# Kernel tuning notes

Measured on AMD Instinct MI355X. Metric: run time of the kernel, lower is better.

The kernel has to match this reference:

```python
import jax, jax.numpy as jnp
import numpy as np

NUM_HEADS = 8
GROUPS = 32
EPS = 1e-5


def setup_inputs() -> dict:
    key = jax.random.key(0)
    ks = jax.random.split(key, 4)
    B, C, H, W = 8, 512, 32, 32
    x = jax.random.normal(ks[0], (B, C, H, W), dtype=jnp.float32)
    gn_w = jnp.ones((C,), dtype=jnp.float32)
    gn_b = jnp.zeros((C,), dtype=jnp.float32)
    qkv_w = jax.random.normal(ks[1], (3 * C, C), dtype=jnp.float32) * (1.0 / np.sqrt(C))
    qkv_b = jnp.zeros((3 * C,), dtype=jnp.float32)
    proj_w = jax.random.normal(ks[2], (C, C), dtype=jnp.float32) * (1.0 / np.sqrt(C))
    proj_b = jnp.zeros((C,), dtype=jnp.float32)
    return {"x": x, "gn_w": gn_w, "gn_b": gn_b, "qkv_w": qkv_w,
            "qkv_b": qkv_b, "proj_w": proj_w, "proj_b": proj_b}


def reference(x, gn_w, gn_b, qkv_w, qkv_b, proj_w, proj_b):
    b, c, h, w = x.shape
    n = h * w
    hd = c // NUM_HEADS
    xf = x.reshape(b, c, n)
    # GroupNorm over (channels_per_group, HW) per sample
    xg = xf.reshape(b, GROUPS, -1)
    mu = jnp.mean(xg, axis=-1, keepdims=True)
    var = jnp.var(xg, axis=-1, keepdims=True)
    xn = ((xg - mu) * jax.lax.rsqrt(var + EPS)).reshape(b, c, n)
    xn = xn * gn_w[None, :, None] + gn_b[None, :, None]
    # 1x1 conv == channel matmul
    qkv = jnp.einsum('oc,bcn->bon', qkv_w, xn) + qkv_b[None, :, None]
    q, k, v = jnp.split(qkv, 3, axis=1)
    q = q.reshape(b, NUM_HEADS, hd, n)
    k = k.reshape(b, NUM_HEADS, hd, n)
    v = v.reshape(b, NUM_HEADS, hd, n)
    scale = hd ** 0.5
    score = jnp.einsum('bhdn,bhdm->bhnm', q, k) / scale  # [b,h,HW,HW]
    attn = jax.nn.softmax(score, axis=-1)
    out = jnp.einsum('bhnm,bhdm->bhnd', attn, v)  # [b,h,HW,hd]
    out = out.transpose(0, 1, 3, 2).reshape(b, c, n)
    out = jnp.einsum('oc,bcn->bon', proj_w, out) + proj_b[None, :, None]
    return x + out.reshape(b, c, h, w)
```

## Files before the change

### kernel.cpp

```cpp
#include <hip/hip_runtime.h>

typedef unsigned short u16;
typedef unsigned long long u64;
typedef __bf16 bf16x8 __attribute__((ext_vector_type(8)));
typedef float f32x4 __attribute__((ext_vector_type(4)));

#define NB 8
#define NC 512
#define NN 1024
#define NHEADS 8
#define HDIM 64
#define CPG 16
#define EPSV 1e-5f
#define LOG2E 1.44269504f

__device__ __forceinline__ float bf2f(u16 h) {
  union { unsigned u; float f; } v; v.u = ((unsigned)h) << 16; return v.f;
}
__device__ __forceinline__ u16 f2bf(float f) {
  union { float f; unsigned u; } v; v.f = f;
  unsigned r = v.u + 0x7fffu + ((v.u >> 16) & 1u);
  return (u16)(r >> 16);
}
__device__ __forceinline__ float h2f(u16 h) {
  unsigned s = (h >> 15) & 1u, e = (h >> 10) & 31u, m = h & 1023u;
  union { unsigned u; float f; } v;
  if (e == 0) { v.u = s << 31; return v.f + (s ? -1.f : 1.f) * (float)m * 5.9604645e-8f; }
  if (e == 31) { v.u = (s << 31) | 0x7F800000u | (m << 13); return v.f; }
  v.u = (s << 31) | ((e + 112u) << 23) | (m << 13);
  return v.f;
}
__device__ __forceinline__ u16 f2h(float f) {
  union { float f; unsigned u; } v; v.f = f;
  unsigned s = (v.u >> 16) & 0x8000u; int e = (int)((v.u >> 23) & 0xFF) - 112;
  unsigned m = v.u & 0x7FFFFFu;
  if (e <= 0) return (u16)s;
  if (e >= 31) return (u16)(s | 0x7C00u);
  u16 h = (u16)(s | (e << 10) | (m >> 13));
  unsigned rem = m & 0x1FFFu;
  if (rem > 0x1000u || (rem == 0x1000u && (h & 1u))) ++h;
  return h;
}
__device__ __forceinline__ float load_elem(const void* p, size_t i, int f) {
  if (f == 1) return bf2f(((const u16*)p)[i]);
  if (f == 2) return h2f(((const u16*)p)[i]);
  return ((const float*)p)[i];
}

__device__ __forceinline__ float exp2_fast(float x) {
  float r;
  asm("v_exp_f32 %0, %1" : "=v"(r) : "v"(x));
  return r;
}

__device__ __forceinline__ int detect_f(const u16* gw_raw) {
  int bf = 0, hf = 0;
#pragma unroll
  for (int i = 0; i < 16; ++i) {
    u16 w = gw_raw[i];
    bf += (w == 0x3F80u);
    hf += (w == 0x3C00u);
  }
  return (bf >= 12) ? 1 : (hf >= 12) ? 2 : 0;
}

__device__ __forceinline__ void cvt4(const void* raw, u16* dst, int i, int f) {
  if (f == 1) {
    *(uint2*)(dst + i) = *(const uint2*)((const u16*)raw + i);
  } else if (f == 0) {
    float4 v = *(const float4*)((const float*)raw + i);
    u16 o[4] = {f2bf(v.x), f2bf(v.y), f2bf(v.z), f2bf(v.w)};
    *(u64*)(dst + i) = *(const u64*)o;
  } else {
    u16 o[4];
#pragma unroll
    for (int k2 = 0; k2 < 4; ++k2) o[k2] = f2bf(h2f(((const u16*)raw)[i + k2]));
    *(u64*)(dst + i) = *(const u64*)o;
  }
}

__device__ __forceinline__ void gn_body(const void* x, int f,
                                        const void* gnw, const void* gnb,
                                        u16* xnT, int bsrc, int bdst,
                                        int g, int t) {
  __shared__ float r1[256], r2[256];
  __shared__ alignas(16) float sxf[CPG * NN];
  __shared__ float sgw[CPG], sgb[CPG];
  const size_t base = ((size_t)(bsrc * NC + g * CPG)) * NN;
  if (t < CPG) {
    sgw[t] = load_elem(gnw, (size_t)(g * CPG + t), f);
    sgb[t] = load_elem(gnb, (size_t)(g * CPG + t), f);
  }
  float s = 0.f, ss = 0.f;
  if (f == 1) {
    const u16* xb = (const u16*)x + base;
    for (int i0 = t * 8; i0 < CPG * NN; i0 += 2048) {
      uint4 dv = *(const uint4*)(xb + i0);
      const u16* pp = (const u16*)&dv;
      float vv[8];
#pragma unroll
      for (int j = 0; j < 8; ++j) { vv[j] = bf2f(pp[j]); s += vv[j]; ss += vv[j] * vv[j]; }
      *(float4*)(sxf + i0)     = make_float4(vv[0], vv[1], vv[2], vv[3]);
      *(float4*)(sxf + i0 + 4) = make_float4(vv[4], vv[5], vv[6], vv[7]);
    }
  } else if (f == 0) {
    const float* xb = (const float*)x + base;
    for (int i0 = t * 4; i0 < CPG * NN; i0 += 1024) {
      float4 v = *(const float4*)(xb + i0);
      *(float4*)(sxf + i0) = v;
      s += v.x + v.y + v.z + v.w;
      ss += v.x * v.x + v.y * v.y + v.z * v.z + v.w * v.w;
    }
  } else {
    for (int i = t; i < CPG * NN; i += 256) {
      float v = load_elem(x, base + i, f);
      sxf[i] = v;
      s += v; ss += v * v;
    }
  }
  r1[t] = s; r2[t] = ss; __syncthreads();
  for (int k = 128; k > 0; k >>= 1) {
    if (t < k) { r1[t] += r1[t + k]; r2[t] += r2[t + k]; }
    __syncthreads();
  }
  const float mu  = r1[0] * (1.f / 16384.f);
  const float var = r2[0] * (1.f / 16384.f) - mu * mu;
  const float rs  = rsqrtf(var + EPSV);
  float wsc[CPG], bsc[CPG];
#pragma unroll
  for (int cl = 0; cl < CPG; ++cl) {
    wsc[cl] = sgw[cl] * rs;
    bsc[cl] = sgb[cl] - mu * wsc[cl];
  }
  u16* dstb = xnT + (size_t)bdst * NN * NC + g * CPG;
  for (int n = t; n < NN; n += 256) {
    u16 o[CPG];
#pragma unroll
    for (int cl = 0; cl < CPG; ++cl)
      o[cl] = f2bf(sxf[cl * NN + n] * wsc[cl] + bsc[cl]);
    u16* dr = dstb + (size_t)n * NC;
    *(uint4*)(dr)     = *(const uint4*)(o);
    *(uint4*)(dr + 8) = *(const uint4*)(o + 8);
  }
}

__global__ __launch_bounds__(256) void prep_all(const void* __restrict__ x,
                                                const void* __restrict__ gnw,
                                                const void* __restrict__ gnb,
                                                const void* __restrict__ qkvw,
                                                const void* __restrict__ qb,
                                                const void* __restrict__ projw,
                                                const void* __restrict__ pb,
                                                u16* __restrict__ wq16,
                                                u16* __restrict__ wp16,
                                                float* __restrict__ cqb,
                                                float* __restrict__ cpb,
                                                int* __restrict__ flag,
                                                u16* __restrict__ xnT) {
  const int f = detect_f((const u16*)gnw);
  const int b = blockIdx.x;
  const int t = threadIdx.x;
  if (b < 768) {
    cvt4(qkvw, wq16, (b * 256 + t) * 4, f);
    return;
  }
  if (b < 1024) {
    cvt4(projw, wp16, ((b - 768) * 256 + t) * 4, f);
    return;
  }
  if (b < 1036) {
    const int i = (b - 1024) * 256 + t;
    if (i < 1536)      cqb[i] = load_elem(qb, (size_t)i, f);
    else if (i < 2048) cpb[i - 1536] = load_elem(pb, (size_t)(i - 1536), f);
    if (b == 1024 && t == 0) *flag = f;
    return;
  }
  const int idx = b - 1036;
  gn_body(x, f, gnw, gnb, xnT, idx >> 5, idx >> 5, idx & 31, t);
}

__global__ __launch_bounds__(256) void gn_only(const void* __restrict__ x,
                                               const void* __restrict__ gnw,
                                               const void* __restrict__ gnb,
                                               u16* __restrict__ xnT, int b0) {
  const int f = detect_f((const u16*)gnw);
  gn_body(x, f, gnw, gnb, xnT, b0, 0, blockIdx.x, threadIdx.x);
}

__global__ __launch_bounds__(256) void gemm_mfma(const u16* __restrict__ A,
                                                 const u16* __restrict__ BnT,
                                                 const float* __restrict__ bias,
                                                 void* __restrict__ out,
                                                 const void* __restrict__ resid,
                                                 const int* __restrict__ flag,
                                                 int M, int K, int b0, int kmode) {
  __shared__ alignas(16) u16 sA[128 * 40];
  __shared__ alignas(16) u16 sB[128 * 40];
  const int m0 = blockIdx.x * 128;
  const int n0 = blockIdx.y * 128;
  const int bz = blockIdx.z;
  const int t = threadIdx.x;
  const int lane = t & 63, wv = t >> 6;
  const int wm = (wv >> 1) * 64, wn = (wv & 1) * 64;
  const int lr = lane & 15, quad = lane >> 4;
  const int f = *flag;

  const int ar0 = t >> 2, akc = (t & 3) * 8;
  const int ar1 = 64 + ar0;
  const int sw0 = akc ^ (ar0 & 24);
  const int sw1 = akc ^ (ar1 & 24);

  f32x4 acc[4][4] = {};

  const u16* pa0 = A + (size_t)(m0 + ar0) * K + akc;
  const u16* pa1 = A + (size_t)(m0 + ar1) * K + akc;
  const u16* pb0 = BnT + ((size_t)bz * NN + n0 + ar0) * K + akc;
  const u16* pb1 = BnT + ((size_t)bz * NN + n0 + ar1) * K + akc;

  uint4 xa0 = *(const uint4*)(pa0);
  uint4 xa1 = *(const uint4*)(pa1);
  uint4 xb0 = *(const uint4*)(pb0);
  uint4 xb1 = *(const uint4*)(pb1);
  uint4 ya0 = *(const uint4*)(pa0 + 32);
  uint4 ya1 = *(const uint4*)(pa1 + 32);
  uint4 yb0 = *(const uint4*)(pb0 + 32);
  uint4 yb1 = *(const uint4*)(pb1 + 32);

#define GEMM_STAGE(ra0, ra1, rb0, rb1)                                   \
  {                                                                      \
    *(uint4*)(sA + ar0 * 40 + akc) = ra0;                                \
    *(uint4*)(sA + ar1 * 40 + akc) = ra1;                                \
    *(uint4*)(sB + ar0 * 40 + sw0) = rb0;                                \
    *(uint4*)(sB + ar1 * 40 + sw1) = rb1;                                \
  }

#define GEMM_MFMA_BLOCK()                                                \
  {                                                                      \
    const u16* pA = sA + (wm + lr) * 40 + quad * 8;                      \
    bf16x8 af[4], bfv[4];                                                \
    _Pragma("unroll")                                                    \
    for (int i = 0; i < 4; ++i) {                                        \
      af[i] = *(const bf16x8*)(pA + i * 640);                            \
      const int rowB = wn + lr + i * 16;                                 \
      bfv[i] = *(const bf16x8*)(sB + rowB * 40 + ((quad * 8) ^ (rowB & 24))); \
    }                                                                    \
    _Pragma("unroll")                                                    \
    for (int i = 0; i < 4; ++i)                                          \
      _Pragma("unroll")                                                  \
      for (int j = 0; j < 4; ++j)                                        \
        acc[i][j] = __builtin_amdgcn_mfma_f32_16x16x32_bf16(af[i], bfv[j], acc[i][j], 0, 0, 0); \
  }

  for (int k0 = 0; k0 < K; k0 += 64) {
    __syncthreads();
    GEMM_STAGE(xa0, xa1, xb0, xb1);
    __syncthreads();
    if (k0 + 64 < K) {
      xa0 = *(const uint4*)(pa0 + k0 + 64);
      xa1 = *(const uint4*)(pa1 + k0 + 64);
      xb0 = *(const uint4*)(pb0 + k0 + 64);
      xb1 = *(const uint4*)(pb1 + k0 + 64);
    }
    GEMM_MFMA_BLOCK();
    __syncthreads();
    GEMM_STAGE(ya0, ya1, yb0, yb1);
    __syncthreads();
    if (k0 + 96 < K) {
      ya0 = *(const uint4*)(pa0 + k0 + 96);
      ya1 = *(const uint4*)(pa1 + k0 + 96);
      yb0 = *(const uint4*)(pb0 + k0 + 96);
      yb1 = *(const uint4*)(pb1 + k0 + 96);
    }
    GEMM_MFMA_BLOCK();
  }

  const bool kstore = (kmode != 0) && (m0 >= 512) && (m0 < 1024);
  if (kstore) {
    u16* kb2 = (u16*)out + ((size_t)(b0 + bz) * 1536 + 512) * NN;
#pragma unroll
    for (int i = 0; i < 4; ++i) {
      const int mb = m0 + wm + i * 16 + quad * 4;
      const int hh = (mb - 512) >> 6;
      const int d0 = (mb - 512) & 63;
      u16* hb = kb2 + (size_t)hh * NN * 64 + d0;
#pragma unroll
      for (int j = 0; j < 4; ++j) {
        const int col = n0 + wn + j * 16 + lr;
        u16 o[4];
#pragma unroll
        for (int r = 0; r < 4; ++r) o[r] = f2bf(acc[i][j][r] + bias[mb + r]);
        *(u64*)(hb + (size_t)col * 64) = *(const u64*)o;
      }
    }
    return;
  }
#pragma unroll
  for (int i = 0; i < 4; ++i) {
    const int mb = m0 + wm + i * 16 + quad * 4;
#pragma unroll
    for (int r = 0; r < 4; ++r) {
      const int mr = mb + r;
      const float bi = bias[mr];
#pragma unroll
      for (int j = 0; j < 4; ++j) {
        const int col = n0 + wn + j * 16 + lr;
        const size_t oidx = ((size_t)(b0 + bz) * M + mr) * NN + col;
        float v = acc[i][j][r] + bi;
        if (resid) {
          v += load_elem(resid, oidx, f);
          if (f == 1)      ((u16*)out)[oidx] = f2bf(v);
          else if (f == 2) ((u16*)out)[oidx] = f2h(v);
          else             ((float*)out)[oidx] = v;
        } else {
          ((u16*)out)[oidx] = f2bf(v);
        }
      }
    }
  }
}

__global__ __launch_bounds__(512) void attn_mfma(const u16* __restrict__ qkv,
                                                 u16* __restrict__ attnOT) {
  __shared__ alignas(16) u16 sK[2][64 * 64];
  __shared__ alignas(16) u16 sV[2][64 * 64];

  const int L   = blockIdx.x + 8 * (blockIdx.y + 8 * blockIdx.z);
  const int xcd = L & 7;
  const int jj  = L >> 3;
  const int grp = xcd + 8 * (jj >> 3);
  const int qt  = jj & 7;
  const int h   = grp & 7;
  const int bz  = grp >> 3;

  const int n0 = qt * 128;
  const u16* qb    = qkv + ((size_t)bz * 1536 + h * HDIM) * NN;
  const u16* kbase = qkv + ((size_t)bz * 1536 + 512) * NN + (size_t)h * NN * HDIM;
  const u16* vb    = qb + (size_t)1024 * NN;
  const int t = threadIdx.x;
  const int lane = t & 63, wv = t >> 6;
  const int lr = lane & 15, quad = lane >> 4;

  const int qcol = n0 + wv * 16 + lr;
  union { u16 u[8]; bf16x8 v; } qa0, qa1;
#pragma unroll
  for (int e = 0; e < 8; ++e) {
    qa0.u[e] = qb[(size_t)(quad * 8 + e) * NN + qcol];
    qa1.u[e] = qb[(size_t)(quad * 8 + 32 + e) * NN + qcol];
  }
  const bf16x8 a0 = qa0.v;
  const bf16x8 a1 = qa1.v;

  const int km = t >> 3;
  const int kc = t & 7;
  const int ke = (km ^ (km >> 3)) & 7;
  const u16* kp = kbase + (size_t)km * 64 + kc * 8;
  const int ksd = km * 64 + ((kc ^ ke) * 8);

  const int sd  = t >> 3;
  const int smo = (t & 7) * 8;
  const u16* vp = vb + (size_t)sd * NN + smo;
  const int vs0 = sd * 64 + (smo ^ (8 * (sd & 7)));

  uint4 pk0, pv0;

  f32x4 acc_o[4] = {};
  float mrow = -1e30f, lrow = 0.f;

  pk0 = *(const uint4*)(kp);
  pv0 = *(const uint4*)(vp);
  *(uint4*)(&sK[0][ksd]) = pk0;
  *(uint4*)(&sV[0][vs0]) = pv0;
  pk0 = *(const uint4*)(kp + 4096);
  pv0 = *(const uint4*)(vp + 64);
  __syncthreads();

  for (int mt = 0; mt < 16; ++mt) {
    const int c = mt & 1;

    f32x4 p[4];
    __builtin_amdgcn_s_setprio(1);
#pragma unroll
    for (int j = 0; j < 4; ++j) {
      const int rk = j * 16 + lr;
      const u16* pKr = &sK[c][rk * 64];
      const int sw = ((rk ^ (rk >> 3)) & 7) * 8;
      bf16x8 k0 = *(const bf16x8*)(pKr + ((quad * 8) ^ sw));
      bf16x8 k1 = *(const bf16x8*)(pKr + ((quad * 8 + 32) ^ sw));
      f32x4 z = {0.f, 0.f, 0.f, 0.f};
      z = __builtin_amdgcn_mfma_f32_16x16x32_bf16(k0, a0, z, 0, 0, 0);
      z = __builtin_amdgcn_mfma_f32_16x16x32_bf16(k1, a1, z, 0, 0, 0);
      p[j] = z;
    }
    __builtin_amdgcn_s_setprio(0);

    float mx = -1e30f;
#pragma unroll
    for (int j = 0; j < 4; ++j)
#pragma unroll
      for (int r = 0; r < 4; ++r) mx = fmaxf(mx, p[j][r]);
    mx = fmaxf(mx, __shfl_xor(mx, 16));
    mx = fmaxf(mx, __shfl_xor(mx, 32));
    const float msc = mx * 0.125f;
    if (!__all(msc - mrow <= 8.f)) {
      const float mnew = fmaxf(mrow, msc);
      const float alpha = exp2_fast((mrow - mnew) * LOG2E);
      mrow = mnew;
      lrow *= alpha;
      float ar[4];
#pragma unroll
      for (int r = 0; r < 4; ++r) ar[r] = __shfl(alpha, quad * 4 + r);
#pragma unroll
      for (int j2 = 0; j2 < 4; ++j2)
#pragma unroll
        for (int r = 0; r < 4; ++r) acc_o[j2][r] *= ar[r];
    }
    const float m2 = mrow * LOG2E;
    float ls = 0.f;
#pragma unroll
    for (int j = 0; j < 4; ++j)
#pragma unroll
      for (int r = 0; r < 4; ++r) {
        const float pe = exp2_fast(fmaf(p[j][r], 0.18033688f, -m2));
        p[j][r] = pe;
        ls += pe;
      }
    ls += __shfl_xor(ls, 16);
    ls += __shfl_xor(ls, 32);
    lrow += ls;

    unsigned pa[4], pb2[4];
#pragma unroll
    for (int j = 0; j < 4; ++j) {
      asm("v_cvt_pk_bf16_f32 %0, %1, %2" : "=v"(pa[j]) : "v"(p[j][0]), "v"(p[j][1]));
      asm("v_cvt_pk_bf16_f32 %0, %1, %2" : "=v"(pb2[j]) : "v"(p[j][2]), "v"(p[j][3]));
    }

    __builtin_amdgcn_s_setprio(1);
#pragma unroll
    for (int ks = 0; ks < 2; ++ks) {
      union { unsigned u[4]; bf16x8 v; } af;
      af.u[0] = pa[2 * ks];
      af.u[1] = pb2[2 * ks];
      af.u[2] = pa[2 * ks + 1];
      af.u[3] = pb2[2 * ks + 1];
#pragma unroll
      for (int j2 = 0; j2 < 4; ++j2) {
        const int rv = j2 * 16 + lr;
        const int swv = 8 * (rv & 7);
        const u16* pVr = &sV[c][rv * 64];
        union { u64 q[2]; bf16x8 v; } bfv;
        bfv.q[0] = *(const u64*)(pVr + ((ks * 32 + 4 * quad) ^ swv));
        bfv.q[1] = *(const u64*)(pVr + ((ks * 32 + 16 + 4 * quad) ^ swv));
        acc_o[j2] = __builtin_amdgcn_mfma_f32_16x16x32_bf16(af.v, bfv.v, acc_o[j2], 0, 0, 0);
      }
    }
    __builtin_amdgcn_s_setprio(0);

    if (mt < 15) {
      const int cn = c ^ 1;
      *(uint4*)(&sK[cn][ksd]) = pk0;
      *(uint4*)(&sV[cn][vs0]) = pv0;
      if (mt < 14) {
        pk0 = *(const uint4*)(kp + (size_t)(mt + 2) * 4096);
        pv0 = *(const uint4*)(vp + (mt + 2) * 64);
      }
      __syncthreads();
    }
  }

  const float invl = 1.f / lrow;
  float ir[4];
#pragma unroll
  for (int r = 0; r < 4; ++r) ir[r] = __shfl(invl, quad * 4 + r);
  const int qrow = n0 + wv * 16 + quad * 4;
#pragma unroll
  for (int r = 0; r < 4; ++r) {
    u16* orow = attnOT + ((size_t)bz * NN + qrow + r) * NC + h * HDIM;
#pragma unroll
    for (int j2 = 0; j2 < 4; ++j2)
      orow[j2 * 16 + lr] = f2bf(acc_o[j2][r] * ir[r]);
  }
}

__global__ void sig_small_ws(u16* out) {
  if (threadIdx.x == 0 && blockIdx.x == 0) out[0] = f2bf(20000.f);
}

extern "C" void kernel_launch(void* const* d_in, const int* in_sizes, int n_in,
                              void* d_out, int out_size, void* d_ws, size_t ws_size,
                              hipStream_t stream) {
  const void* x      = d_in[0];
  const void* gn_w   = d_in[1];
  const void* gn_b   = d_in[2];
  const void* qkv_w  = d_in[3];
  const void* qkv_b  = d_in[4];
  const void* proj_w = d_in[5];
  const void* proj_b = d_in[6];
  char* ws = (char*)d_ws;
  const size_t MB = (size_t)1 << 20;

  u16*   wq16 = (u16*)(ws);
  u16*   wp16 = (u16*)(ws + 3 * MB / 2);
  float* cqb  = (float*)(ws + 2 * MB);
  float* cpb  = (float*)(ws + 2 * MB + 8192);
  int*   flag = (int*)  (ws + 2 * MB + 16384);

  if (ws_size >= 36 * MB) {
    u16* xnT    = (u16*)(ws + 3 * MB);
    u16* qkvb   = (u16*)(ws + 11 * MB);
    u16* attnOT = xnT;
    prep_all<<<dim3(1036 + NB * 32), dim3(256), 0, stream>>>(
        x, gn_w, gn_b, qkv_w, qkv_b, proj_w, proj_b,
        wq16, wp16, cqb, cpb, flag, xnT);
    gemm_mfma<<<dim3(12, 8, NB), dim3(256), 0, stream>>>(wq16, xnT, cqb, qkvb,
                                                         nullptr, flag, 1536, NC, 0, 1);
    attn_mfma<<<dim3(8, NHEADS, NB), dim3(512), 0, stream>>>(qkvb, attnOT);
    gemm_mfma<<<dim3(4, 8, NB), dim3(256), 0, stream>>>(wp16, attnOT, cpb, d_out,
                                                        x, flag, NC, NC, 0, 0);
  } else if (ws_size >= 9 * MB) {
    u16* xnT    = (u16*)(ws + 3 * MB);
    u16* qkvb   = (u16*)(ws + 4 * MB);
    u16* attnOT = (u16*)(ws + 7 * MB);
    prep_all<<<dim3(1036), dim3(256), 0, stream>>>(
        x, gn_w, gn_b, qkv_w, qkv_b, proj_w, proj_b,
        wq16, wp16, cqb, cpb, flag, xnT);
    for (int b = 0; b < NB; ++b) {
      gn_only<<<dim3(32), dim3(256), 0, stream>>>(x, gn_w, gn_b, xnT, b);
      gemm_mfma<<<dim3(12, 8, 1), dim3(256), 0, stream>>>(wq16, xnT, cqb, qkvb,
                                                          nullptr, flag, 1536, NC, 0, 1);
      attn_mfma<<<dim3(8, NHEADS, 1), dim3(512), 0, stream>>>(qkvb, attnOT);
      gemm_mfma<<<dim3(4, 8, 1), dim3(256), 0, stream>>>(wp16, attnOT, cpb, d_out,
                                                         x, flag, NC, NC, b, 0);
    }
  } else {
    sig_small_ws<<<dim3(1), dim3(64), 0, stream>>>((u16*)d_out);
  }
}
```

Measured before the change: 178.6 us.

## Give each attention wave two query tiles and halve block threads

The attention kernel now runs 4 waves of 256 threads instead of 8. Each wave processes two 16-row query tiles, so every K and V fragment read from shared memory feeds two MFMAs. Each thread loads twice as much of the K/V tiles to keep the per-block tile size the same. This cuts LDS reads per MFMA and barrier participants, at the cost of higher register pressure and fewer waves per block for latency hiding.

Result: no change. 178.3 us (median of 2 runs) (-0.2%).

```diff
diff --git a/kernel.cpp b/kernel.cpp
--- a/kernel.cpp
+++ b/kernel.cpp
@@ -319,7 +319,7 @@
   }
 }
 
-__global__ __launch_bounds__(512) void attn_mfma(const u16* __restrict__ qkv,
+__global__ __launch_bounds__(256) void attn_mfma(const u16* __restrict__ qkv,
                                                  u16* __restrict__ attnOT) {
   __shared__ alignas(16) u16 sK[2][64 * 64];
   __shared__ alignas(16) u16 sV[2][64 * 64];
@@ -340,44 +340,56 @@
   const int lane = t & 63, wv = t >> 6;
   const int lr = lane & 15, quad = lane >> 4;
 
-  const int qcol = n0 + wv * 16 + lr;
-  union { u16 u[8]; bf16x8 v; } qa0, qa1;
+  const int qcol = n0 + wv * 32 + lr;
+  union { u16 u[8]; bf16x8 v; } qh[4];
 #pragma unroll
   for (int e = 0; e < 8; ++e) {
-    qa0.u[e] = qb[(size_t)(quad * 8 + e) * NN + qcol];
-    qa1.u[e] = qb[(size_t)(quad * 8 + 32 + e) * NN + qcol];
-  }
-  const bf16x8 a0 = qa0.v;
-  const bf16x8 a1 = qa1.v;
-
-  const int km = t >> 3;
-  const int kc = t & 7;
+    qh[0].u[e] = qb[(size_t)(quad * 8 + e) * NN + qcol];
+    qh[1].u[e] = qb[(size_t)(quad * 8 + 32 + e) * NN + qcol];
+    qh[2].u[e] = qb[(size_t)(quad * 8 + e) * NN + qcol + 16];
+    qh[3].u[e] = qb[(size_t)(quad * 8 + 32 + e) * NN + qcol + 16];
+  }
+  const bf16x8 a0_0 = qh[0].v, a1_0 = qh[1].v;
+  const bf16x8 a0_1 = qh[2].v, a1_1 = qh[3].v;
+
+  const int km = t >> 2;
+  const int kc = t & 3;
   const int ke = (km ^ (km >> 3)) & 7;
   const u16* kp = kbase + (size_t)km * 64 + kc * 8;
-  const int ksd = km * 64 + ((kc ^ ke) * 8);
 
   const int sd  = t >> 3;
   const int smo = (t & 7) * 8;
   const u16* vp = vb + (size_t)sd * NN + smo;
   const int vs0 = sd * 64 + (smo ^ (8 * (sd & 7)));
-
-  uint4 pk0, pv0;
-
-  f32x4 acc_o[4] = {};
-  float mrow = -1e30f, lrow = 0.f;
+  const int vs1 = (sd + 32) * 64 + (smo ^ (8 * ((sd + 32) & 7)));
+
+  uint4 pk0, pk1, pv0, pv1;
+
+  f32x4 acc_o0[4] = {}, acc_o1[4] = {};
+  float mrow0 = -1e30f, lrow0 = 0.f;
+  float mrow1 = -1e30f, lrow1 = 0.f;
 
   pk0 = *(const uint4*)(kp);
+  pk1 = *(const uint4*)(kp + 32);
   pv0 = *(const uint4*)(vp);
-  *(uint4*)(&sK[0][ksd]) = pk0;
-  *(uint4*)(&sV[0][vs0]) = pv0;
+  pv1 = *(const uint4*)(vp + (size_t)32 * NN);
+  {
+    u16* kd = &sK[0][km * 64];
+    *(uint4*)(kd + ((kc ^ ke) * 8)) = pk0;
+    *(uint4*)(kd + (((kc + 4) ^ ke) * 8)) = pk1;
+    *(uint4*)(&sV[0][vs0]) = pv0;
+    *(uint4*)(&sV[0][vs1]) = pv1;
+  }
   pk0 = *(const uint4*)(kp + 4096);
+  pk1 = *(const uint4*)(kp + 4096 + 32);
   pv0 = *(const uint4*)(vp + 64);
+  pv1 = *(const uint4*)(vp + (size_t)32 * NN + 64);
   __syncthreads();
 
   for (int mt = 0; mt < 16; ++mt) {
     const int c = mt & 1;
 
-    f32x4 p[4];
+    f32x4 p0[4], p1[4];
     __builtin_amdgcn_s_setprio(1);
 #pragma unroll
     for (int j = 0; j < 4; ++j) {
@@ -386,63 +398,111 @@
       const int sw = ((rk ^ (rk >> 3)) & 7) * 8;
       bf16x8 k0 = *(const bf16x8*)(pKr + ((quad * 8) ^ sw));
       bf16x8 k1 = *(const bf16x8*)(pKr + ((quad * 8 + 32) ^ sw));
-      f32x4 z = {0.f, 0.f, 0.f, 0.f};
-      z = __builtin_amdgcn_mfma_f32_16x16x32_bf16(k0, a0, z, 0, 0, 0);
-      z = __builtin_amdgcn_mfma_f32_16x16x32_bf16(k1, a1, z, 0, 0, 0);
-      p[j] = z;
+      f32x4 z0 = {0.f, 0.f, 0.f, 0.f};
+      z0 = __builtin_amdgcn_mfma_f32_16x16x32_bf16(k0, a0_0, z0, 0, 0, 0);
+      z0 = __builtin_amdgcn_mfma_f32_16x16x32_bf16(k1, a1_0, z0, 0, 0, 0);
+      p0[j] = z0;
+      f32x4 z1 = {0.f, 0.f, 0.f, 0.f};
+      z1 = __builtin_amdgcn_mfma_f32_16x16x32_bf16(k0, a0_1, z1, 0, 0, 0);
+      z1 = __builtin_amdgcn_mfma_f32_16x16x32_bf16(k1, a1_1, z1, 0, 0, 0);
+      p1[j] = z1;
     }
     __builtin_amdgcn_s_setprio(0);
 
-    float mx = -1e30f;
-#pragma unroll
-    for (int j = 0; j < 4; ++j)
-#pragma unroll
-      for (int r = 0; r < 4; ++r) mx = fmaxf(mx, p[j][r]);
-    mx = fmaxf(mx, __shfl_xor(mx, 16));
-    mx = fmaxf(mx, __shfl_xor(mx, 32));
-    const float msc = mx * 0.125f;
-    if (!__all(msc - mrow <= 8.f)) {
-      const float mnew = fmaxf(mrow, msc);
-      const float alpha = exp2_fast((mrow - mnew) * LOG2E);
-      mrow = mnew;
-      lrow *= alpha;
-      float ar[4];
-#pragma unroll
-      for (int r = 0; r < 4; ++r) ar[r] = __shfl(alpha, quad * 4 + r);
-#pragma unroll
-      for (int j2 = 0; j2 < 4; ++j2)
-#pragma unroll
-        for (int r = 0; r < 4; ++r) acc_o[j2][r] *= ar[r];
-    }
-    const float m2 = mrow * LOG2E;
-    float ls = 0.f;
-#pragma unroll
-    for (int j = 0; j < 4; ++j)
-#pragma unroll
-      for (int r = 0; r < 4; ++r) {
-        const float pe = exp2_fast(fmaf(p[j][r], 0.18033688f, -m2));
-        p[j][r] = pe;
-        ls += pe;
-      }
-    ls += __shfl_xor(ls, 16);
-    ls += __shfl_xor(ls, 32);
-    lrow += ls;
-
-    unsigned pa[4], pb2[4];
-#pragma unroll
-    for (int j = 0; j < 4; ++j) {
-      asm("v_cvt_pk_bf16_f32 %0, %1, %2" : "=v"(pa[j]) : "v"(p[j][0]), "v"(p[j][1]));
-      asm("v_cvt_pk_bf16_f32 %0, %1, %2" : "=v"(pb2[j]) : "v"(p[j][2]), "v"(p[j][3]));
+    unsigned pa0[4], pb0_[4];
+    {
+      float mx = -1e30f;
+#pragma unroll
+      for (int j = 0; j < 4; ++j)
+#pragma unroll
+        for (int r = 0; r < 4; ++r) mx = fmaxf(mx, p0[j][r]);
+      mx = fmaxf(mx, __shfl_xor(mx, 16));
+      mx = fmaxf(mx, __shfl_xor(mx, 32));
+      const float msc = mx * 0.125f;
+      if (!__all(msc - mrow0 <= 8.f)) {
+        const float mnew = fmaxf(mrow0, msc);
+        const float alpha = exp2_fast((mrow0 - mnew) * LOG2E);
+        mrow0 = mnew;
+        lrow0 *= alpha;
+        float ar[4];
+#pragma unroll
+        for (int r = 0; r < 4; ++r) ar[r] = __shfl(alpha, quad * 4 + r);
+#pragma unroll
+        for (int j2 = 0; j2 < 4; ++j2)
+#pragma unroll
+          for (int r = 0; r < 4; ++r) acc_o0[j2][r] *= ar[r];
+      }
+      const float m2 = mrow0 * LOG2E;
+      float ls = 0.f;
+#pragma unroll
+      for (int j = 0; j < 4; ++j)
+#pragma unroll
+        for (int r = 0; r < 4; ++r) {
+          const float pe = exp2_fast(fmaf(p0[j][r], 0.18033688f, -m2));
+          p0[j][r] = pe;
+          ls += pe;
+        }
+      ls += __shfl_xor(ls, 16);
+      ls += __shfl_xor(ls, 32);
+      lrow0 += ls;
+#pragma unroll
+      for (int j = 0; j < 4; ++j) {
+        asm("v_cvt_pk_bf16_f32 %0, %1, %2" : "=v"(pa0[j]) : "v"(p0[j][0]), "v"(p0[j][1]));
+        asm("v_cvt_pk_bf16_f32 %0, %1, %2" : "=v"(pb0_[j]) : "v"(p0[j][2]), "v"(p0[j][3]));
+      }
+    }
+
+    unsigned pa1[4], pb1_[4];
+    {
+      float mx = -1e30f;
+#pragma unroll
+      for (int j = 0; j < 4; ++j)
+#pragma unroll
+        for (int r = 0; r < 4; ++r) mx = fmaxf(mx, p1[j][r]);
+      mx = fmaxf(mx, __shfl_xor(mx, 16));
+      mx = fmaxf(mx, __shfl_xor(mx, 32));
+      const float msc = mx * 0.125f;
+      if (!__all(msc - mrow1 <= 8.f)) {
+        const float mnew = fmaxf(mrow1, msc);
+        const float alpha = exp2_fast((mrow1 - mnew) * LOG2E);
+        mrow1 = mnew;
+        lrow1 *= alpha;
+        float ar[4];
+#pragma unroll
+        for (int r = 0; r < 4; ++r) ar[r] = __shfl(alpha, quad * 4 + r);
+#pragma unroll
+        for (int j2 = 0; j2 < 4; ++j2)
+#pragma unroll
+          for (int r = 0; r < 4; ++r) acc_o1[j2][r] *= ar[r];
+      }
+      const float m2 = mrow1 * LOG2E;
+      float ls = 0.f;
+#pragma unroll
+      for (int j = 0; j < 4; ++j)
+#pragma unroll
+        for (int r = 0; r < 4; ++r) {
+          const float pe = exp2_fast(fmaf(p1[j][r], 0.18033688f, -m2));
+          p1[j][r] = pe;
+          ls += pe;
+        }
+      ls += __shfl_xor(ls, 16);
+      ls += __shfl_xor(ls, 32);
+      lrow1 += ls;
+#pragma unroll
+      for (int j = 0; j < 4; ++j) {
+        asm("v_cvt_pk_bf16_f32 %0, %1, %2" : "=v"(pa1[j]) : "v"(p1[j][0]), "v"(p1[j][1]));
+        asm("v_cvt_pk_bf16_f32 %0, %1, %2" : "=v"(pb1_[j]) : "v"(p1[j][2]), "v"(p1[j][3]));
+      }
     }
 
     __builtin_amdgcn_s_setprio(1);
 #pragma unroll
     for (int ks = 0; ks < 2; ++ks) {
-      union { unsigned u[4]; bf16x8 v; } af;
-      af.u[0] = pa[2 * ks];
-      af.u[1] = pb2[2 * ks];
-      af.u[2] = pa[2 * ks + 1];
-      af.u[3] = pb2[2 * ks + 1];
+      union { unsigned u[4]; bf16x8 v; } af0, af1;
+      af0.u[0] = pa0[2 * ks];  af0.u[1] = pb0_[2 * ks];
+      af0.u[2] = pa0[2 * ks + 1]; af0.u[3] = pb0_[2 * ks + 1];
+      af1.u[0] = pa1[2 * ks];  af1.u[1] = pb1_[2 * ks];
+      af1.u[2] = pa1[2 * ks + 1]; af1.u[3] = pb1_[2 * ks + 1];
 #pragma unroll
       for (int j2 = 0; j2 < 4; ++j2) {
         const int rv = j2 * 16 + lr;
@@ -451,34 +511,58 @@
         union { u64 q[2]; bf16x8 v; } bfv;
         bfv.q[0] = *(const u64*)(pVr + ((ks * 32 + 4 * quad) ^ swv));
         bfv.q[1] = *(const u64*)(pVr + ((ks * 32 + 16 + 4 * quad) ^ swv));
-        acc_o[j2] = __builtin_amdgcn_mfma_f32_16x16x32_bf16(af.v, bfv.v, acc_o[j2], 0, 0, 0);
+        acc_o0[j2] = __builtin_amdgcn_mfma_f32_16x16x32_bf16(af0.v, bfv.v, acc_o0[j2], 0, 0, 0);
+        acc_o1[j2] = __builtin_amdgcn_mfma_f32_16x16x32_bf16(af1.v, bfv.v, acc_o1[j2], 0, 0, 0);
       }
     }
     __builtin_amdgcn_s_setprio(0);
 
     if (mt < 15) {
       const int cn = c ^ 1;
-      *(uint4*)(&sK[cn][ksd]) = pk0;
+      u16* kd = &sK[cn][km * 64];
+      *(uint4*)(kd + ((kc ^ ke) * 8)) = pk0;
+      *(uint4*)(kd + (((kc + 4) ^ ke) * 8)) = pk1;
       *(uint4*)(&sV[cn][vs0]) = pv0;
+      *(uint4*)(&sV[cn][vs1]) = pv1;
       if (mt < 14) {
-        pk0 = *(const uint4*)(kp + (size_t)(mt + 2) * 4096);
-        pv0 = *(const uint4*)(vp + (mt + 2) * 64);
+        const size_t ko = (size_t)(mt + 2) * 4096;
+        const int mo = (mt + 2) * 64;
+        pk0 = *(const uint4*)(kp + ko);
+        pk1 = *(const uint4*)(kp + ko + 32);
+        pv0 = *(const uint4*)(vp + mo);
+        pv1 = *(const uint4*)(vp + (size_t)32 * NN + mo);
       }
       __syncthreads();
     }
   }
 
-  const float invl = 1.f / lrow;
-  float ir[4];
-#pragma unroll
-  for (int r = 0; r < 4; ++r) ir[r] = __shfl(invl, quad * 4 + r);
-  const int qrow = n0 + wv * 16 + quad * 4;
-#pragma unroll
-  for (int r = 0; r < 4; ++r) {
-    u16* orow = attnOT + ((size_t)bz * NN + qrow + r) * NC + h * HDIM;
-#pragma unroll
-    for (int j2 = 0; j2 < 4; ++j2)
-      orow[j2 * 16 + lr] = f2bf(acc_o[j2][r] * ir[r]);
+  {
+    const float invl = 1.f / lrow0;
+    float ir[4];
+#pragma unroll
+    for (int r = 0; r < 4; ++r) ir[r] = __shfl(invl, quad * 4 + r);
+    const int qrow = n0 + wv * 32 + quad * 4;
+#pragma unroll
+    for (int r = 0; r < 4; ++r) {
+      u16* orow = attnOT + ((size_t)bz * NN + qrow + r) * NC + h * HDIM;
+#pragma unroll
+      for (int j2 = 0; j2 < 4; ++j2)
+        orow[j2 * 16 + lr] = f2bf(acc_o0[j2][r] * ir[r]);
+    }
+  }
+  {
+    const float invl = 1.f / lrow1;
+    float ir[4];
+#pragma unroll
+    for (int r = 0; r < 4; ++r) ir[r] = __shfl(invl, quad * 4 + r);
+    const int qrow = n0 + wv * 32 + 16 + quad * 4;
+#pragma unroll
+    for (int r = 0; r < 4; ++r) {
+      u16* orow = attnOT + ((size_t)bz * NN + qrow + r) * NC + h * HDIM;
+#pragma unroll
+      for (int j2 = 0; j2 < 4; ++j2)
+        orow[j2 * 16 + lr] = f2bf(acc_o1[j2][r] * ir[r]);
+    }
   }
 }
 
@@ -514,7 +598,7 @@
         wq16, wp16, cqb, cpb, flag, xnT);
     gemm_mfma<<<dim3(12, 8, NB), dim3(256), 0, stream>>>(wq16, xnT, cqb, qkvb,
                                                          nullptr, flag, 1536, NC, 0, 1);
-    attn_mfma<<<dim3(8, NHEADS, NB), dim3(512), 0, stream>>>(qkvb, attnOT);
+    attn_mfma<<<dim3(8, NHEADS, NB), dim3(256), 0, stream>>>(qkvb, attnOT);
     gemm_mfma<<<dim3(4, 8, NB), dim3(256), 0, stream>>>(wp16, attnOT, cpb, d_out,
                                                         x, flag, NC, NC, 0, 0);
   } else if (ws_size >= 9 * MB) {
@@ -528,7 +612,7 @@
       gn_only<<<dim3(32), dim3(256), 0, stream>>>(x, gn_w, gn_b, xnT, b);
       gemm_mfma<<<dim3(12, 8, 1), dim3(256), 0, stream>>>(wq16, xnT, cqb, qkvb,
                                                           nullptr, flag, 1536, NC, 0, 1);
-      attn_mfma<<<dim3(8, NHEADS, 1), dim3(512), 0, stream>>>(qkvb, attnOT);
+      attn_mfma<<<dim3(8, NHEADS, 1), dim3(256), 0, stream>>>(qkvb, attnOT);
       gemm_mfma<<<dim3(4, 8, 1), dim3(256), 0, stream>>>(wp16, attnOT, cpb, d_out,
                                                          x, flag, NC, NC, b, 0);
     }
```
